# Kernel optimization log

Measured on AMD Instinct MI355X. Metric: run time of the kernel, lower is better.

The kernel has to match this reference:

```python
import jax, jax.numpy as jnp
import numpy as np

N, E, G, IN, H, L, C = 20000, 320000, 128, 16, 64, 4, 10
AVG_D_LOG = float(np.log(17.0))  # log(avg_degree + 1)


def setup_inputs() -> dict:
    key = jax.random.key(0)
    ks = jax.random.split(key, 24)
    p = lambda k, shape: jax.random.normal(k, shape, dtype=jnp.float32) * 0.05
    return dict(
        h=jax.random.normal(ks[0], (N, IN), jnp.float32),
        snorm_n=jax.random.uniform(ks[1], (N, 1), jnp.float32, 0.05, 1.0),
        embW=p(ks[2], (IN, H)), embB=p(ks[3], (H,)),
        preW=p(ks[4], (L, 2 * H, H)), preB=p(ks[5], (L, H)),
        postW=p(ks[6], (L, 13 * H, H)), postB=p(ks[7], (L, H)),
        mixW=p(ks[8], (L, H, H)), mixB=p(ks[9], (L, H)),
        r1W=p(ks[10], (H, H // 2)), r1B=p(ks[11], (H // 2,)),
        r2W=p(ks[12], (H // 2, H // 4)), r2B=p(ks[13], (H // 4,)),
        r3W=p(ks[14], (H // 4, C)), r3B=p(ks[15], (C,)),
        src=jax.random.randint(ks[16], (E,), 0, N),
        dst=jax.random.randint(ks[17], (E,), 0, N),
        graph_ids=jnp.sort(jax.random.randint(ks[18], (N,), 0, G)),
    )


def _pna_forward(h, snorm_n, embW, embB, preW, preB, postW, postB, mixW, mixB,
                 r1W, r1B, r2W, r2B, r3W, r3B, src, dst, graph_ids):
    # Degree-based scalers (computed once; graph is fixed across layers)
    deg = jax.ops.segment_sum(jnp.ones((E,), h.dtype), dst, num_segments=N)  # [N]
    degc = jnp.maximum(deg, 1.0)[:, None]
    logd = jnp.log(deg + 1.0)
    amp = (logd / AVG_D_LOG)[:, None]                      # amplification scaler
    att = (AVG_D_LOG / jnp.maximum(logd, 1e-5))[:, None]   # attenuation scaler
    has_nb = (deg > 0.0)[:, None]

    x = h @ embW + embB  # node embedding [N, H]
    for i in range(L):
        x_in = x
        # pretrans: per-edge message from cat(h_src, h_dst)  [E, H]
        m = jnp.concatenate([x[src], x[dst]], axis=-1) @ preW[i] + preB[i]
        # multi-aggregator reduce at dst: mean, max, min, std
        mean = jax.ops.segment_sum(m, dst, num_segments=N) / degc
        msq = jax.ops.segment_sum(m * m, dst, num_segments=N) / degc
        std = jnp.sqrt(jax.nn.relu(msq - mean * mean) + 1e-5)
        mx = jnp.where(has_nb, jax.ops.segment_max(m, dst, num_segments=N), 0.0)
        mn = jnp.where(has_nb, jax.ops.segment_min(m, dst, num_segments=N), 0.0)
        agg = jnp.concatenate([mean, mx, mn, std], axis=-1)  # [N, 4H]
        # degree scalers: identity, amplification, attenuation -> [N, 12H]
        scaled = jnp.concatenate([agg, agg * amp, agg * att], axis=-1)
        # posttrans over cat(scaled_agg, h) -> [N, H]
        y = jnp.concatenate([scaled, x], axis=-1) @ postW[i] + postB[i]
        # tower mixing network (LeakyReLU FC)
        y = jax.nn.leaky_relu(y @ mixW[i] + mixB[i])
        y = y * snorm_n          # graph norm
        x = x_in + y             # residual
    # mean-nodes readout per graph
    gsum = jax.ops.segment_sum(x, graph_ids, num_segments=G)
    cnt = jnp.maximum(jax.ops.segment_sum(jnp.ones((N,), x.dtype), graph_ids, num_segments=G), 1.0)
    hg = gsum / cnt[:, None]
    # MLPReadout: two halving ReLU layers + classifier
    hg = jax.nn.relu(hg @ r1W + r1B)
    hg = jax.nn.relu(hg @ r2W + r2B)
    return hg @ r3W + r3B  # [G, C]


def reference(h, snorm_n, embW, embB, preW, preB, postW, postB, mixW, mixB,
              r1W, r1B, r2W, r2B, r3W, r3B, src, dst, graph_ids):
    return _pna_forward(h, snorm_n, embW, embB, preW, preB, postW, postB,
                        mixW, mixB, r1W, r1B, r2W, r2B, r3W, r3B,
                        src, dst, graph_ids)
```

## Files before the change

### kernel.cpp

```cpp
#include <hip/hip_runtime.h>
#include <math.h>

#define N_ 20000
#define E_ 320000
#define G_ 128
#define IN_ 16
#define H_ 64
#define L_ 4
#define C_ 10
#define AVG_D_LOG 2.8332133440562162f

union F4 { float4 v; float f[4]; };

typedef _Float16 h8 __attribute__((ext_vector_type(8)));
typedef _Float16 h4 __attribute__((ext_vector_type(4)));
typedef float f4x __attribute__((ext_vector_type(4)));
#define MFMA16(a, b, c) __builtin_amdgcn_mfma_f32_16x16x32_f16((a), (b), (c), 0, 0, 0)


__global__ __launch_bounds__(256) void k_setup(
    const float* __restrict__ h, const float* __restrict__ embW, const float* __restrict__ embB,
    float* __restrict__ x,
    const float* __restrict__ preW, const float* __restrict__ postW, const float* __restrict__ mixW,
    _Float16* __restrict__ preWT, _Float16* __restrict__ postWT, _Float16* __restrict__ mixWT,
    int* __restrict__ zbase) {
  __shared__ float tl[64][68];
  int bb = blockIdx.x, tid = threadIdx.x;
  if (bb < 5000) {
    int n = bb * 4 + (tid >> 6);
    int c = tid & 63;
    float acc = embB[c];
#pragma unroll
    for (int k = 0; k < IN_; k++) acc += h[n * IN_ + k] * embW[k * H_ + c];
    x[n * H_ + c] = acc;
  } else if (bb < 5052) {
    int t = bb - 5000;
    int l = t / 13, kt = t % 13, k0 = kt * 64;
    const float* Wsrc = postW + (size_t)l * 53248;
    _Float16* Wdst = postWT + (size_t)l * 53248;
    int r = tid >> 4, q4 = (tid & 15) * 4;
#pragma unroll
    for (int p = 0; p < 4; p++) {
      int rr = p * 16 + r;
      float4 v = *(const float4*)(Wsrc + (size_t)(k0 + rr) * 64 + q4);
      tl[rr][q4 + 0] = v.x; tl[rr][q4 + 1] = v.y;
      tl[rr][q4 + 2] = v.z; tl[rr][q4 + 3] = v.w;
    }
    __syncthreads();
#pragma unroll
    for (int p = 0; p < 4; p++) {
      int o = p * 256 + tid;
      int c = o >> 4, j4 = (o & 15) * 4;
      h4 hv;
      hv[0] = (_Float16)tl[j4 + 0][c]; hv[1] = (_Float16)tl[j4 + 1][c];
      hv[2] = (_Float16)tl[j4 + 2][c]; hv[3] = (_Float16)tl[j4 + 3][c];
      *(h4*)(Wdst + (size_t)c * 832 + k0 + j4) = hv;
    }
  } else if (bb < 5244) {
    int idx = (bb - 5052) * 256 + tid;
    if (idx < 32768) {
      int l = idx >> 13, r = idx & 8191;
      int c = r >> 6, k = r & 63;
      preWT[idx] = (_Float16)preW[l * 8192 + k * 64 + c];
    } else {
      int j = idx - 32768;
      int l = j >> 12, r = j & 4095;
      int c = r >> 6, k = r & 63;
      mixWT[j] = (_Float16)mixW[l * 4096 + k * 64 + c];
    }
  } else {
    int i = (bb - 5244) * 256 + tid;
    if (i < 2 * N_) zbase[i] = 0;
  }
}


__global__ __launch_bounds__(256) void k_hist(const int* __restrict__ dst, int* __restrict__ deg) {
  int e = blockIdx.x * 256 + threadIdx.x;
  if (e < E_) atomicAdd(&deg[dst[e]], 1);
}


__global__ __launch_bounds__(1024) void k_scan(const int* __restrict__ deg, int* __restrict__ offs) {
  __shared__ int sh[1024];
  int t = threadIdx.x;
  int base = t * 20;
  int local[20];
  int s = 0;
  if (t < 1000) {
#pragma unroll
    for (int c = 0; c < 5; c++) {
      int4 v = *(const int4*)(deg + base + c * 4);
      local[c * 4 + 0] = s; s += v.x;
      local[c * 4 + 1] = s; s += v.y;
      local[c * 4 + 2] = s; s += v.z;
      local[c * 4 + 3] = s; s += v.w;
    }
  }
  sh[t] = s;
  __syncthreads();
  for (int off = 1; off < 1024; off <<= 1) {
    int v = (t >= off) ? sh[t - off] : 0;
    __syncthreads();
    sh[t] += v;
    __syncthreads();
  }
  if (t < 1000) {
    int excl = sh[t] - s;
#pragma unroll
    for (int c = 0; c < 5; c++) {
      int4 o;
      o.x = excl + local[c * 4 + 0];
      o.y = excl + local[c * 4 + 1];
      o.z = excl + local[c * 4 + 2];
      o.w = excl + local[c * 4 + 3];
      *(int4*)(offs + base + c * 4) = o;
    }
  }
  if (t == 0) offs[N_] = sh[1023];
}


__global__ __launch_bounds__(256) void k_mix(
    const int* __restrict__ src, const int* __restrict__ dst,
    const int* __restrict__ offs, int* __restrict__ cursor, int* __restrict__ csr,
    const int* __restrict__ deg,
    float* __restrict__ ampv, float* __restrict__ attv,
    float* __restrict__ invd, float* __restrict__ hnb,
    const float* __restrict__ x, const _Float16* __restrict__ preWT,
    const float* __restrict__ preB, _Float16* __restrict__ ah, float* __restrict__ b) {
  int bb = blockIdx.x, tid = threadIdx.x;
  if (bb < 1250) {
    int e = bb * 256 + tid;
    if (e < E_) {
      int d = dst[e];
      int pos = offs[d] + atomicAdd(&cursor[d], 1);
      csr[pos] = src[e];
    }
  } else if (bb < 1329) {
    int idx = (bb - 1250) * 256 + tid;
    if (idx < N_) {
      float d = (float)deg[idx];
      float logd = logf(d + 1.f);
      ampv[idx] = logd / AVG_D_LOG;
      attv[idx] = AVG_D_LOG / fmaxf(logd, 1e-5f);
      invd[idx] = 1.f / fmaxf(d, 1.f);
      hnb[idx] = d > 0.f ? 1.f : 0.f;
    }
  } else {
    int n0 = (bb - 1329) * 32;
    int lane = tid & 63, wv = tid >> 6;
    int mt = wv & 1, nh = wv >> 1;
    int l15 = lane & 15, k0q = (lane >> 4) * 8;
    int mrow = n0 + mt * 16 + l15;
    const float* xr = x + (size_t)mrow * 64;
    const _Float16* wb0 = preWT + (size_t)(nh * 64 + l15) * 64 + k0q;
    f4x acc0 = {0.f,0.f,0.f,0.f}, acc1 = {0.f,0.f,0.f,0.f}, acc2 = {0.f,0.f,0.f,0.f}, acc3 = {0.f,0.f,0.f,0.f};
#pragma unroll
    for (int kb = 0; kb < 64; kb += 32) {
      int ko = kb + k0q;
      F4 xa, xb2;
      xa.v = *(const float4*)(xr + ko);
      xb2.v = *(const float4*)(xr + ko + 4);
      h8 af;
      af[0]=(_Float16)xa.f[0]; af[1]=(_Float16)xa.f[1]; af[2]=(_Float16)xa.f[2]; af[3]=(_Float16)xa.f[3];
      af[4]=(_Float16)xb2.f[0]; af[5]=(_Float16)xb2.f[1]; af[6]=(_Float16)xb2.f[2]; af[7]=(_Float16)xb2.f[3];
      acc0 = MFMA16(af, *(const h8*)(wb0 + kb), acc0);
      acc1 = MFMA16(af, *(const h8*)(wb0 + 1024 + kb), acc1);
      acc2 = MFMA16(af, *(const h8*)(wb0 + 2048 + kb), acc2);
      acc3 = MFMA16(af, *(const h8*)(wb0 + 3072 + kb), acc3);
    }
    int rbase = n0 + mt * 16 + (lane >> 4) * 4;
    f4x accs[4] = {acc0, acc1, acc2, acc3};
#pragma unroll
    for (int t = 0; t < 4; t++) {
      int col = nh * 64 + t * 16 + l15;
#pragma unroll
      for (int r = 0; r < 4; r++) {
        int n = rbase + r;
        if (col < 64) ah[(size_t)n * 64 + col] = (_Float16)accs[t][r];
        else          b[(size_t)n * 64 + (col - 64)] = accs[t][r] + preB[col - 64];
      }
    }
  }
}


__global__ __launch_bounds__(256, 5) void k_layer(
    const _Float16* __restrict__ ahin, const float* __restrict__ bin,
    const int* __restrict__ offs, const int* __restrict__ csr,
    const float* __restrict__ invd, const float* __restrict__ hnb,
    const _Float16* __restrict__ WT, const float* __restrict__ Bv,
    const _Float16* __restrict__ mixWT, const float* __restrict__ mixB,
    const float* __restrict__ ampv, const float* __restrict__ attv,
    const float* __restrict__ snorm, float* __restrict__ x,
    const _Float16* __restrict__ preWT, const float* __restrict__ preB,
    _Float16* __restrict__ ahout, float* __restrict__ bout, int do_pre) {
  __shared__ _Float16 aggs[16 * 280];
  __shared__ _Float16 ys[16 * 88];
  __shared__ _Float16 xs[16 * 88];
  __shared__ _Float16 xt[16 * 88];
  __shared__ float xs32[16 * 68];
  __shared__ int csr_s[1024];
  __shared__ int soffs[17];
  __shared__ float scal[48];
  int tid = threadIdx.x;
  int n0 = blockIdx.x * 16;
  int lane = tid & 63, wv = tid >> 6;

  int e0 = offs[n0];
  int ecnt = offs[n0 + 16] - e0;
  {
    int row = tid >> 4, qq = tid & 15;
    F4 xv; xv.v = *(const float4*)(x + (size_t)(n0 + row) * 64 + qq * 4);
    h4 xh;
    xh[0] = (_Float16)xv.f[0]; xh[1] = (_Float16)xv.f[1];
    xh[2] = (_Float16)xv.f[2]; xh[3] = (_Float16)xv.f[3];
    *(h4*)(xt + row * 88 + qq * 4) = xh;
    *(float4*)(xs32 + row * 68 + qq * 4) = xv.v;
  }
  if (tid < 17) soffs[tid] = offs[n0 + tid];
  if (tid >= 32 && tid < 48) {
    int i = tid - 32;
    scal[i] = ampv[n0 + i];
    scal[16 + i] = attv[n0 + i];
    scal[32 + i] = snorm[n0 + i];
  }
  int nlA = tid >> 4, qA = tid & 15;
  F4 bv; bv.v = *(const float4*)(bin + (size_t)(n0 + nlA) * 64 + qA * 4);
  float inv = invd[n0 + nlA], hn = hnb[n0 + nlA];
  int col0 = wv * 16 + (tid & 15);
  float b0v = Bv[col0];
  float mb0 = mixB[col0];
  {
    int cnt = ecnt < 1024 ? ecnt : 1024;
    for (int i = tid; i < cnt; i += 256) csr_s[i] = csr[e0 + i];
  }
  __syncthreads();

  {
    int nl = nlA, q = qA;
    int o0 = soffs[nl];
    int deg = soffs[nl + 1] - o0;
    float sum[4], sq[4], mx[4], mn[4];
#pragma unroll
    for (int i = 0; i < 4; i++) {
      sum[i] = 0.f; sq[i] = 0.f;
      mx[i] = -__builtin_inff(); mn[i] = __builtin_inff();
    }
#define GLD_(S) (*(const h4*)(ahin + (size_t)(S) * 64 + q * 4))
#define PROC1_(AV)                                                       \
    do {                                                                 \
      _Pragma("unroll")                                                  \
      for (int i = 0; i < 4; i++) {                                      \
        float v0 = (float)AV[i];                                         \
        sum[i] += v0; sq[i] += v0 * v0;                                  \
        mx[i] = fmaxf(mx[i], v0); mn[i] = fminf(mn[i], v0);              \
      }                                                                  \
    } while (0)
    if (ecnt <= 1024) {
      int lo = o0 - e0;
      int j = 0;
      h4 A0, A1, A2, A3;
      if (j + 3 < deg) {
        A0 = GLD_(csr_s[lo]);     A1 = GLD_(csr_s[lo + 1]);
        A2 = GLD_(csr_s[lo + 2]); A3 = GLD_(csr_s[lo + 3]);
      }
      for (; j + 7 < deg; j += 4) {
        int s0 = csr_s[lo + j + 4], s1 = csr_s[lo + j + 5];
        int s2 = csr_s[lo + j + 6], s3 = csr_s[lo + j + 7];
        h4 B0 = GLD_(s0), B1 = GLD_(s1), B2 = GLD_(s2), B3 = GLD_(s3);
        PROC1_(A0); PROC1_(A1); PROC1_(A2); PROC1_(A3);
        A0 = B0; A1 = B1; A2 = B2; A3 = B3;
      }
      if (j + 3 < deg) { PROC1_(A0); PROC1_(A1); PROC1_(A2); PROC1_(A3); j += 4; }
      for (; j < deg; j++) { h4 a0 = GLD_(csr_s[lo + j]); PROC1_(a0); }
    } else {
      int j = 0;
      for (; j < deg; j++) { h4 a0 = GLD_(csr[o0 + j]); PROC1_(a0); }
    }
#undef GLD_
#undef PROC1_
    h4 hm, hx, hmn, hs;
#pragma unroll
    for (int i = 0; i < 4; i++) {
      float mean_a = sum[i] * inv;
      float var = sq[i] * inv - mean_a * mean_a;
      hs[i] = (_Float16)sqrtf(fmaxf(var, 0.f) + 1e-5f);
      bool nb = hn > 0.5f;
      hm[i] = (_Float16)(nb ? (mean_a + bv.f[i]) : 0.f);
      hx[i] = (_Float16)(nb ? (mx[i] + bv.f[i]) : 0.f);
      hmn[i] = (_Float16)(nb ? (mn[i] + bv.f[i]) : 0.f);
    }
    _Float16* ap = aggs + nl * 280 + q * 4;
    *(h4*)(ap) = hm;
    *(h4*)(ap + 64) = hx;
    *(h4*)(ap + 128) = hmn;
    *(h4*)(ap + 192) = hs;
  }
  __syncthreads();

  int l15 = lane & 15, k0q = (lane >> 4) * 8;
  const _Float16* ag = aggs + (size_t)l15 * 280 + k0q;
  const _Float16* w0 = WT + (size_t)col0 * 832 + k0q;
  f4x aI = {0.f,0.f,0.f,0.f}, aA = {0.f,0.f,0.f,0.f}, aT = {0.f,0.f,0.f,0.f};
#pragma unroll 4
  for (int kb = 0; kb < 256; kb += 32) {
    h8 af = *(const h8*)(ag + kb);
    aI = MFMA16(af, *(const h8*)(w0 + kb), aI);
    aA = MFMA16(af, *(const h8*)(w0 + 256 + kb), aA);
    aT = MFMA16(af, *(const h8*)(w0 + 512 + kb), aT);
  }
  const _Float16* xtr = xt + (size_t)l15 * 88 + k0q;
#pragma unroll
  for (int kb = 0; kb < 64; kb += 32) {
    h8 af = *(const h8*)(xtr + kb);
    aI = MFMA16(af, *(const h8*)(w0 + 768 + kb), aI);
  }
  int qr = (lane >> 4) * 4;
  int rbase = n0 + qr;
#pragma unroll
  for (int r = 0; r < 4; r++) {
    float amp = scal[qr + r], att = scal[16 + qr + r];
    ys[(qr + r) * 88 + col0] = (_Float16)(aI[r] + b0v + amp * aA[r] + att * aT[r]);
  }
  __syncthreads();
  f4x m0 = {0.f,0.f,0.f,0.f};
  const _Float16* yr = ys + (size_t)l15 * 88 + k0q;
  const _Float16* mw0 = mixWT + (size_t)col0 * 64 + k0q;
#pragma unroll
  for (int kb = 0; kb < 64; kb += 32) {
    h8 af = *(const h8*)(yr + kb);
    m0 = MFMA16(af, *(const h8*)(mw0 + kb), m0);
  }
#pragma unroll
  for (int r = 0; r < 4; r++) {
    int n = rbase + r;
    float sn = scal[32 + qr + r];
    float t0 = m0[r] + mb0; t0 = t0 > 0.f ? t0 : 0.01f * t0;
    float xo0 = xs32[(qr + r) * 68 + col0] + t0 * sn;
    x[(size_t)n * 64 + col0] = xo0;
    xs[(qr + r) * 88 + col0] = (_Float16)xo0;
  }

  if (do_pre) {
    __syncthreads();
    int ch = wv;
    const _Float16* xf = xs + (size_t)l15 * 88 + k0q;
    const _Float16* wb0 = preWT + (size_t)(ch * 32 + l15) * 64 + k0q;
    f4x p0 = {0.f,0.f,0.f,0.f}, p1 = {0.f,0.f,0.f,0.f};
#pragma unroll
    for (int kb = 0; kb < 64; kb += 32) {
      h8 af = *(const h8*)(xf + kb);
      p0 = MFMA16(af, *(const h8*)(wb0 + kb), p0);
      p1 = MFMA16(af, *(const h8*)(wb0 + 1024 + kb), p1);
    }
    int prb = n0 + (lane >> 4) * 4;
    f4x accs[2] = {p0, p1};
#pragma unroll
    for (int t = 0; t < 2; t++) {
      int col = ch * 32 + t * 16 + l15;
#pragma unroll
      for (int r = 0; r < 4; r++) {
        int n = prb + r;
        if (col < 64) ahout[(size_t)n * 64 + col] = (_Float16)accs[t][r];
        else          bout[(size_t)n * 64 + (col - 64)] = accs[t][r] + preB[col - 64];
      }
    }
  }
}


__device__ inline int lower_bound_gid(const int* __restrict__ gid, int val) {
  int lo = 0, hi = N_;
  while (lo < hi) {
    int mid = (lo + hi) >> 1;
    if (gid[mid] < val) lo = mid + 1; else hi = mid;
  }
  return lo;
}

__global__ __launch_bounds__(512) void k_readout_fused(
    const float* __restrict__ x, const int* __restrict__ gid,
    const float* __restrict__ r1W, const float* __restrict__ r1B,
    const float* __restrict__ r2W, const float* __restrict__ r2B,
    const float* __restrict__ r3W, const float* __restrict__ r3B,
    float* __restrict__ out) {
  __shared__ float part[8 * 64];
  __shared__ float hg[64];
  __shared__ float t1[32];
  __shared__ float t2[16];
  int g = blockIdx.x, tid = threadIdx.x;
  int lo = lower_bound_gid(gid, g);
  int hi = lower_bound_gid(gid, g + 1);
  int c = tid & 63, w = tid >> 6;
  float s = 0.f;
  for (int n = lo + w; n < hi; n += 8) s += x[(size_t)n * 64 + c];
  part[w * 64 + c] = s;
  __syncthreads();
  if (w == 0) {
    float tot = 0.f;
#pragma unroll
    for (int p = 0; p < 8; p++) tot += part[p * 64 + c];
    float cnt = (float)(hi - lo);
    if (cnt < 1.f) cnt = 1.f;
    hg[c] = tot / cnt;
  }
  __syncthreads();
  if (tid < 32) {
    float acc = r1B[tid];
#pragma unroll 8
    for (int k = 0; k < 64; k++) acc += hg[k] * r1W[k * 32 + tid];
    t1[tid] = fmaxf(acc, 0.f);
  }
  __syncthreads();
  if (tid < 16) {
    float acc = r2B[tid];
#pragma unroll 8
    for (int k = 0; k < 32; k++) acc += t1[k] * r2W[k * 16 + tid];
    t2[tid] = fmaxf(acc, 0.f);
  }
  __syncthreads();
  if (tid < 10) {
    float acc = r3B[tid];
#pragma unroll
    for (int k = 0; k < 16; k++) acc += t2[k] * r3W[k * 10 + tid];
    out[g * 10 + tid] = acc;
  }
}


extern "C" void kernel_launch(void* const* d_in, const int* in_sizes, int n_in,
                              void* d_out, int out_size, void* d_ws, size_t ws_size,
                              hipStream_t stream) {
  const float* h     = (const float*)d_in[0];
  const float* snorm = (const float*)d_in[1];
  const float* embW  = (const float*)d_in[2];
  const float* embB  = (const float*)d_in[3];
  const float* preW  = (const float*)d_in[4];
  const float* preB  = (const float*)d_in[5];
  const float* postW = (const float*)d_in[6];
  const float* postB = (const float*)d_in[7];
  const float* mixW  = (const float*)d_in[8];
  const float* mixB  = (const float*)d_in[9];
  const float* r1W   = (const float*)d_in[10];
  const float* r1B   = (const float*)d_in[11];
  const float* r2W   = (const float*)d_in[12];
  const float* r2B   = (const float*)d_in[13];
  const float* r3W   = (const float*)d_in[14];
  const float* r3B   = (const float*)d_in[15];
  const int* src     = (const int*)d_in[16];
  const int* dst     = (const int*)d_in[17];
  const int* gid     = (const int*)d_in[18];
  float* out = (float*)d_out;

  char* w = (char*)d_ws;
  float* x        = (float*)w; w += (size_t)N_ * 64 * 4;
  _Float16* ah0   = (_Float16*)w; w += (size_t)N_ * 64 * 2;
  _Float16* ah1   = (_Float16*)w; w += (size_t)N_ * 64 * 2;
  float* b0       = (float*)w; w += (size_t)N_ * 64 * 4;
  float* b1       = (float*)w; w += (size_t)N_ * 64 * 4;
  _Float16* preWT = (_Float16*)w; w += (size_t)4 * 128 * 64 * 2;
  _Float16* postWT= (_Float16*)w; w += (size_t)4 * 64 * 832 * 2;
  _Float16* mixWT = (_Float16*)w; w += (size_t)4 * 64 * 64 * 2;
  float* ampv = (float*)w; w += (size_t)N_ * 4;
  float* attv = (float*)w; w += (size_t)N_ * 4;
  float* invd = (float*)w; w += (size_t)N_ * 4;
  float* hnb  = (float*)w; w += (size_t)N_ * 4;
  int* csr    = (int*)w;   w += (size_t)E_ * 4;
  int* offs   = (int*)w;   w += (size_t)(N_ + 64) * 4;
  int* zbase  = (int*)w;
  int* deg    = (int*)w;   w += (size_t)N_ * 4;
  int* cursor = (int*)w;   w += (size_t)N_ * 4;

  k_setup<<<5401, 256, 0, stream>>>(h, embW, embB, x, preW, postW, mixW,
                                    preWT, postWT, mixWT, zbase);
  k_hist<<<E_ / 256, 256, 0, stream>>>(dst, deg);
  k_scan<<<1, 1024, 0, stream>>>(deg, offs);
  k_mix<<<1250 + 79 + 625, 256, 0, stream>>>(src, dst, offs, cursor, csr, deg,
                                             ampv, attv, invd, hnb,
                                             x, preWT, preB, ah0, b0);
  int gb = N_ / 16;
  _Float16* ahs[2] = {ah0, ah1};
  float* bs[2] = {b0, b1};
  for (int l = 0; l < L_; l++) {
    int pin = l & 1, pout = 1 - pin;
    k_layer<<<gb, 256, 0, stream>>>(ahs[pin], bs[pin], offs, csr, invd, hnb,
                                    postWT + (size_t)l * 53248, postB + l * H_,
                                    mixWT + (size_t)l * 4096, mixB + l * H_,
                                    ampv, attv, snorm, x,
                                    preWT + (size_t)(l + 1 < L_ ? l + 1 : 0) * 8192,
                                    preB + (l + 1 < L_ ? l + 1 : 0) * H_,
                                    ahs[pout], bs[pout], l + 1 < L_ ? 1 : 0);
  }
  k_readout_fused<<<G_, 512, 0, stream>>>(x, gid, r1W, r1B, r2W, r2B, r3W, r3B, out);
}
```

Baseline: 273.8 us.

## Fold histogram into setup and scan into mix kernel, zero via memset

Moves the degree histogram into the setup kernel, which runs after a hipMemsetAsync that zeroes deg and cursor. The scan now shares a launch with the scaler computation and the first pre-transform GEMM (four 256-thread sub-tiles per 1024-thread block), and the CSR scatter becomes its own kernel. The aim is to drop a kernel launch and the serialised single-block scan. In exchange, the scan block now overlaps other work, and the pre-transform GEMM runs in 1024-thread blocks.

```diff
diff --git a/kernel.cpp b/kernel.cpp
--- a/kernel.cpp
+++ b/kernel.cpp
@@ -23,7 +23,7 @@
     float* __restrict__ x,
     const float* __restrict__ preW, const float* __restrict__ postW, const float* __restrict__ mixW,
     _Float16* __restrict__ preWT, _Float16* __restrict__ postWT, _Float16* __restrict__ mixWT,
-    int* __restrict__ zbase) {
+    const int* __restrict__ dst, int* __restrict__ deg) {
   __shared__ float tl[64][68];
   int bb = blockIdx.x, tid = threadIdx.x;
   if (bb < 5000) {
@@ -69,76 +69,58 @@
       mixWT[j] = (_Float16)mixW[l * 4096 + k * 64 + c];
     }
   } else {
-    int i = (bb - 5244) * 256 + tid;
-    if (i < 2 * N_) zbase[i] = 0;
-  }
-}
-
-
-__global__ __launch_bounds__(256) void k_hist(const int* __restrict__ dst, int* __restrict__ deg) {
-  int e = blockIdx.x * 256 + threadIdx.x;
-  if (e < E_) atomicAdd(&deg[dst[e]], 1);
-}
-
-
-__global__ __launch_bounds__(1024) void k_scan(const int* __restrict__ deg, int* __restrict__ offs) {
-  __shared__ int sh[1024];
-  int t = threadIdx.x;
-  int base = t * 20;
-  int local[20];
-  int s = 0;
-  if (t < 1000) {
-#pragma unroll
-    for (int c = 0; c < 5; c++) {
-      int4 v = *(const int4*)(deg + base + c * 4);
-      local[c * 4 + 0] = s; s += v.x;
-      local[c * 4 + 1] = s; s += v.y;
-      local[c * 4 + 2] = s; s += v.z;
-      local[c * 4 + 3] = s; s += v.w;
-    }
-  }
-  sh[t] = s;
-  __syncthreads();
-  for (int off = 1; off < 1024; off <<= 1) {
-    int v = (t >= off) ? sh[t - off] : 0;
-    __syncthreads();
-    sh[t] += v;
-    __syncthreads();
-  }
-  if (t < 1000) {
-    int excl = sh[t] - s;
-#pragma unroll
-    for (int c = 0; c < 5; c++) {
-      int4 o;
-      o.x = excl + local[c * 4 + 0];
-      o.y = excl + local[c * 4 + 1];
-      o.z = excl + local[c * 4 + 2];
-      o.w = excl + local[c * 4 + 3];
-      *(int4*)(offs + base + c * 4) = o;
-    }
-  }
-  if (t == 0) offs[N_] = sh[1023];
-}
-
-
-__global__ __launch_bounds__(256) void k_mix(
-    const int* __restrict__ src, const int* __restrict__ dst,
-    const int* __restrict__ offs, int* __restrict__ cursor, int* __restrict__ csr,
-    const int* __restrict__ deg,
+    int e = (bb - 5244) * 256 + tid;
+    if (e < E_) atomicAdd(&deg[dst[e]], 1);
+  }
+}
+
+
+__global__ __launch_bounds__(1024) void k_scan(
+    const int* __restrict__ deg, int* __restrict__ offs,
     float* __restrict__ ampv, float* __restrict__ attv,
     float* __restrict__ invd, float* __restrict__ hnb,
     const float* __restrict__ x, const _Float16* __restrict__ preWT,
     const float* __restrict__ preB, _Float16* __restrict__ ah, float* __restrict__ b) {
-  int bb = blockIdx.x, tid = threadIdx.x;
-  if (bb < 1250) {
-    int e = bb * 256 + tid;
-    if (e < E_) {
-      int d = dst[e];
-      int pos = offs[d] + atomicAdd(&cursor[d], 1);
-      csr[pos] = src[e];
-    }
-  } else if (bb < 1329) {
-    int idx = (bb - 1250) * 256 + tid;
+  int bx = blockIdx.x, tid = threadIdx.x;
+  if (bx == 0) {
+    __shared__ int sh[1024];
+    int t = tid;
+    int base = t * 20;
+    int local[20];
+    int s = 0;
+    if (t < 1000) {
+#pragma unroll
+      for (int c = 0; c < 5; c++) {
+        int4 v = *(const int4*)(deg + base + c * 4);
+        local[c * 4 + 0] = s; s += v.x;
+        local[c * 4 + 1] = s; s += v.y;
+        local[c * 4 + 2] = s; s += v.z;
+        local[c * 4 + 3] = s; s += v.w;
+      }
+    }
+    sh[t] = s;
+    __syncthreads();
+    for (int off = 1; off < 1024; off <<= 1) {
+      int v = (t >= off) ? sh[t - off] : 0;
+      __syncthreads();
+      sh[t] += v;
+      __syncthreads();
+    }
+    if (t < 1000) {
+      int excl = sh[t] - s;
+#pragma unroll
+      for (int c = 0; c < 5; c++) {
+        int4 o;
+        o.x = excl + local[c * 4 + 0];
+        o.y = excl + local[c * 4 + 1];
+        o.z = excl + local[c * 4 + 2];
+        o.w = excl + local[c * 4 + 3];
+        *(int4*)(offs + base + c * 4) = o;
+      }
+    }
+    if (t == 0) offs[N_] = sh[1023];
+  } else if (bx < 21) {
+    int idx = (bx - 1) * 1024 + tid;
     if (idx < N_) {
       float d = (float)deg[idx];
       float logd = logf(d + 1.f);
@@ -148,8 +130,11 @@
       hnb[idx] = d > 0.f ? 1.f : 0.f;
     }
   } else {
-    int n0 = (bb - 1329) * 32;
-    int lane = tid & 63, wv = tid >> 6;
+    int sub = tid >> 8;
+    int t2 = tid & 255;
+    int n0 = (bx - 21) * 128 + sub * 32;
+    if (n0 >= N_) return;
+    int lane = t2 & 63, wv = t2 >> 6;
     int mt = wv & 1, nh = wv >> 1;
     int l15 = lane & 15, k0q = (lane >> 4) * 8;
     int mrow = n0 + mt * 16 + l15;
@@ -182,6 +167,18 @@
         else          b[(size_t)n * 64 + (col - 64)] = accs[t][r] + preB[col - 64];
       }
     }
+  }
+}
+
+
+__global__ __launch_bounds__(256) void k_scatter(
+    const int* __restrict__ src, const int* __restrict__ dst,
+    const int* __restrict__ offs, int* __restrict__ cursor, int* __restrict__ csr) {
+  int e = blockIdx.x * 256 + threadIdx.x;
+  if (e < E_) {
+    int d = dst[e];
+    int pos = offs[d] + atomicAdd(&cursor[d], 1);
+    csr[pos] = src[e];
   }
 }
 
@@ -473,13 +470,12 @@
   int* deg    = (int*)w;   w += (size_t)N_ * 4;
   int* cursor = (int*)w;   w += (size_t)N_ * 4;
 
-  k_setup<<<5401, 256, 0, stream>>>(h, embW, embB, x, preW, postW, mixW,
-                                    preWT, postWT, mixWT, zbase);
-  k_hist<<<E_ / 256, 256, 0, stream>>>(dst, deg);
-  k_scan<<<1, 1024, 0, stream>>>(deg, offs);
-  k_mix<<<1250 + 79 + 625, 256, 0, stream>>>(src, dst, offs, cursor, csr, deg,
-                                             ampv, attv, invd, hnb,
-                                             x, preWT, preB, ah0, b0);
+  hipMemsetAsync(zbase, 0, (size_t)2 * N_ * 4, stream);
+  k_setup<<<6494, 256, 0, stream>>>(h, embW, embB, x, preW, postW, mixW,
+                                    preWT, postWT, mixWT, dst, deg);
+  k_scan<<<178, 1024, 0, stream>>>(deg, offs, ampv, attv, invd, hnb,
+                                   x, preWT, preB, ah0, b0);
+  k_scatter<<<1250, 256, 0, stream>>>(src, dst, offs, cursor, csr);
   int gb = N_ / 16;
   _Float16* ahs[2] = {ah0, ah1};
   float* bs[2] = {b0, b1};
```

New measurement: 268.7 us. Within noise of the previous version (-1.9%).
